# Kernel optimization log

Hardware: AMD Instinct MI355X
Metric: run time of the kernel (lower is better)

The kernel has to match this reference:

```python
import jax, jax.numpy as jnp
from jax import lax
import numpy as np

B, T, F, K = 64, 512, 1024, 64


def setup_inputs() -> dict:
    key = jax.random.key(0)
    ks = jax.random.split(key, 7)
    text_vec = jax.random.normal(ks[0], (B, T, F), dtype=jnp.float32)
    # variable-length mask; first timestep always on (torchcrf requirement)
    lengths = jax.random.randint(ks[1], (B,), T // 2, T + 1)
    mask = jnp.arange(T)[None, :] < lengths[:, None]  # [B,T] bool
    W = jax.random.normal(ks[2], (K, F), dtype=jnp.float32) * 0.02
    b = jnp.zeros((K,), dtype=jnp.float32)
    start_transitions = jax.random.uniform(ks[3], (K,), minval=-0.1, maxval=0.1)
    end_transitions = jax.random.uniform(ks[4], (K,), minval=-0.1, maxval=0.1)
    transitions = jax.random.uniform(ks[5], (K, K), minval=-0.1, maxval=0.1)
    return dict(text_vec=text_vec, mask=mask, W=W, b=b,
                start_transitions=start_transitions,
                end_transitions=end_transitions,
                transitions=transitions)


def _viterbi_decode(emission, mask, start, end, trans):
    """emission [N,T,K] float, mask [N,T] bool -> best tags [N,T] int32.
    Faithful masked Viterbi (torchcrf semantics); padded positions carry the
    last valid tag forward."""
    N, Tlen, Ktags = emission.shape
    score0 = start[None, :] + emission[:, 0]  # [N,K]
    idx_id = jnp.broadcast_to(jnp.arange(Ktags), (N, Ktags))

    def step(score, xs):
        e_t, m_t = xs  # [N,K], [N]
        cand = score[:, :, None] + trans[None, :, :] + e_t[:, None, :]  # [N,Kprev,Knext]
        new_score = jnp.max(cand, axis=1)
        best_prev = jnp.argmax(cand, axis=1)  # [N,K]
        new_score = jnp.where(m_t[:, None], new_score, score)
        best_prev = jnp.where(m_t[:, None], best_prev, idx_id)
        return new_score, best_prev

    xs = (jnp.swapaxes(emission[:, 1:], 0, 1), mask[:, 1:].T)  # time-major
    final_score, hist = lax.scan(step, score0, xs)  # hist [T-1,N,K]
    final_score = final_score + end[None, :]
    last_tag = jnp.argmax(final_score, axis=-1)  # [N]

    def back(tag, h_t):
        prev = jnp.take_along_axis(h_t, tag[:, None], axis=1)[:, 0]
        return prev, tag

    first_tag, tags_rest = lax.scan(back, last_tag, hist, reverse=True)
    tags = jnp.concatenate([first_tag[None, :], tags_rest], axis=0).T  # [N,T]
    return tags.astype(jnp.int32)


def reference(text_vec, mask, W, b, start_transitions, end_transitions, transitions):
    # cal_emission: Linear then reshape [B,T,K] -> [B,1,T,K]
    em = jnp.einsum('btf,kf->btk', text_vec, W) + b  # [B,T,K]
    emission = em[:, None, :, :]  # [B,1,T,K]
    # decode: flatten the singleton dim and run Viterbi
    em_flat = emission.reshape(-1, T, K)  # [B*1,T,K]
    mask_flat = jnp.broadcast_to(mask[:, None, :], (B, 1, T)).reshape(-1, T)
    pred = _viterbi_decode(em_flat, mask_flat, start_transitions,
                           end_transitions, transitions)
    pred = pred.reshape(B, 1, T)
    return emission, pred
```

## Files before the change

kernel.cpp:

```cpp
#include <hip/hip_runtime.h>
#include <hip/hip_bf16.h>

#define BB 64
#define TT 512
#define FF 1024
#define KK 64

typedef unsigned char uchar;
typedef float float2v __attribute__((ext_vector_type(2)));

#define BM 64
#define BF 64
#define LDA 68

__global__ __launch_bounds__(256)
void emission_kernel(const float* __restrict__ X, const float* __restrict__ W,
                     const float* __restrict__ bias, float* __restrict__ em)
{
    __shared__ float As[BF][LDA];
    __shared__ float Bs[BF][LDA];
    const int tid = threadIdx.x;
    const int row0 = blockIdx.x * BM;
    const int tm = tid & 15;
    const int tn = tid >> 4;
    const int lq = tid & 15;
    const int lr = tid >> 4;

    float acc[4][4];
#pragma unroll
    for (int i = 0; i < 4; ++i)
#pragma unroll
        for (int jj = 0; jj < 4; ++jj) acc[i][jj] = 0.f;

    for (int f0 = 0; f0 < FF; f0 += BF) {
#pragma unroll
        for (int p = 0; p < 4; ++p) {
            const int r = p * 16 + lr;
            float4 a = *(const float4*)(X + (size_t)(row0 + r) * FF + f0 + lq * 4);
            As[lq * 4 + 0][r] = a.x;
            As[lq * 4 + 1][r] = a.y;
            As[lq * 4 + 2][r] = a.z;
            As[lq * 4 + 3][r] = a.w;
            float4 w = *(const float4*)(W + (size_t)r * FF + f0 + lq * 4);
            Bs[lq * 4 + 0][r] = w.x;
            Bs[lq * 4 + 1][r] = w.y;
            Bs[lq * 4 + 2][r] = w.z;
            Bs[lq * 4 + 3][r] = w.w;
        }
        __syncthreads();
#pragma unroll
        for (int f = 0; f < BF; ++f) {
            float4 a = *(const float4*)&As[f][tm * 4];
            float4 b = *(const float4*)&Bs[f][tn * 4];
            acc[0][0] += a.x * b.x; acc[0][1] += a.x * b.y; acc[0][2] += a.x * b.z; acc[0][3] += a.x * b.w;
            acc[1][0] += a.y * b.x; acc[1][1] += a.y * b.y; acc[1][2] += a.y * b.z; acc[1][3] += a.y * b.w;
            acc[2][0] += a.z * b.x; acc[2][1] += a.z * b.y; acc[2][2] += a.z * b.z; acc[2][3] += a.z * b.w;
            acc[3][0] += a.w * b.x; acc[3][1] += a.w * b.y; acc[3][2] += a.w * b.z; acc[3][3] += a.w * b.w;
        }
        __syncthreads();
    }

    const float4 b4 = *(const float4*)(bias + tn * 4);
#pragma unroll
    for (int i = 0; i < 4; ++i) {
        float4 o;
        o.x = acc[i][0] + b4.x;
        o.y = acc[i][1] + b4.y;
        o.z = acc[i][2] + b4.z;
        o.w = acc[i][3] + b4.w;
        *(float4*)(em + (size_t)(row0 + tm * 4 + i) * KK + tn * 4) = o;
    }
}

#define VSTEP(EV, TIDX) do {                                                   \
    const float2v* sp2 = (const float2v*)&sbuf[(TIDX) & 1][0];                 \
    float m_;                                                                  \
    _Pragma("unroll")                                                          \
    for (int c = 0; c < 8; ++c) {                                              \
        const float2v p0 = sp2[c * 4 + 0] + tc2[c * 4 + 0];                    \
        const float2v p1 = sp2[c * 4 + 1] + tc2[c * 4 + 1];                    \
        const float2v p2 = sp2[c * 4 + 2] + tc2[c * 4 + 2];                    \
        const float2v p3 = sp2[c * 4 + 3] + tc2[c * 4 + 3];                    \
        const float ma = fmaxf(fmaxf(p0.x, p0.y), p1.x);           \
        const float mb = fmaxf(fmaxf(p1.y, p2.x), p2.y);                       \
        const float mc = fmaxf(fmaxf(p3.x, p3.y), ma);                         \
        const float w_ = fmaxf(mb, mc);                                        \
        m_ = (c == 0) ? w_ : fmaxf(m_, w_);                                    \
    }                                                                          \
    score = m_ + (EV);                                                         \
    sbuf[((TIDX) + 1) & 1][j] = score;       \
    sb[(size_t)(TIDX) * KK + j] = score;                                       \
} while (0)

#define RLANE(I) __uint_as_float((unsigned)__builtin_amdgcn_readlane((int)__float_as_uint(score), (I)))

__global__ __launch_bounds__(64)
__attribute__((amdgpu_waves_per_eu(1, 1)))
void viterbi_fwd(const float* __restrict__ em, const void* __restrict__ maskp,
                 const float* __restrict__ startT, const float* __restrict__ endT,
                 const float* __restrict__ trans, float* __restrict__ shist,
                 int* __restrict__ btarr)
{
    __shared__ float sbuf[2][KK];

    const int b = blockIdx.x;
    const int j = threadIdx.x;

    const uchar* m8 = (const uchar*)maskp;
    const int* m32 = (const int*)maskp;
    const bool u8m = (m8[1] != 0);

    int myc;
    if (u8m) {
        const uint2 mv = *(const uint2*)(m8 + (size_t)b * TT + j * 8);
        const unsigned s4 = (mv.x & 0x01010101u) + (mv.y & 0x01010101u);
        myc = (int)((s4 * 0x01010101u) >> 24);
    } else {
        const int* mp = m32 + (size_t)b * TT + j * 8;
        const int4 a = *(const int4*)mp;
        const int4 c = *(const int4*)(mp + 4);
        myc = (a.x != 0) + (a.y != 0) + (a.z != 0) + (a.w != 0)
            + (c.x != 0) + (c.y != 0) + (c.z != 0) + (c.w != 0);
    }
#pragma unroll
    for (int o = 1; o < 64; o <<= 1) myc += __shfl_xor(myc, o, 64);
    const int len = myc;

    float2v tc2[32];
#pragma unroll
    for (int i = 0; i < 32; ++i) {
        tc2[i].x = trans[(2 * i) * KK + j];
        tc2[i].y = trans[(2 * i + 1) * KK + j];
    }
#pragma unroll
    for (int i = 0; i < 32; ++i) asm volatile("" : "+v"(tc2[i]));

    const float* emb = em + (size_t)b * TT * KK;
    float* sb = shist + (size_t)b * TT * KK;

    float score = startT[j] + emb[j];
    sb[j] = score;
    sbuf[1][j] = score;

    float eA = emb[1 * KK + j];
    float eB = emb[2 * KK + j];
    float eC = emb[3 * KK + j];
    float eD = emb[4 * KK + j];

    int t = 1;
    for (; t + 3 < len; t += 4) {
        VSTEP(eA, t);     eA = emb[(size_t)((t + 4 < TT) ? t + 4 : TT - 1) * KK + j];
        VSTEP(eB, t + 1); eB = emb[(size_t)((t + 5 < TT) ? t + 5 : TT - 1) * KK + j];
        VSTEP(eC, t + 2); eC = emb[(size_t)((t + 6 < TT) ? t + 6 : TT - 1) * KK + j];
        VSTEP(eD, t + 3); eD = emb[(size_t)((t + 7 < TT) ? t + 7 : TT - 1) * KK + j];
    }
    for (; t < len; ++t) {
        VSTEP(eA, t);
        eA = eB; eB = eC; eC = eD;
    }

    score += endT[j];
    float bm = -__builtin_inff();
    int bt = 0;
#pragma unroll
    for (int i = 0; i < KK; ++i) {
        const float si = RLANE(i);
        if (si > bm) { bm = si; bt = i; }
    }
    if (j == 0) btarr[b] = bt;
}

__global__ __launch_bounds__(256)
void hist_kernel(const float* __restrict__ em, const void* __restrict__ maskp,
                 const float* __restrict__ trans, const float* __restrict__ shist,
                 uchar* __restrict__ histg)
{
    const int tid = threadIdx.x;
    const int bid = blockIdx.x;
    const int b = bid >> 6;
    const int t0 = (bid & 63) * 8;

    __shared__ float tl[64][65];
    __shared__ float srow[8][64];

    const uchar* m8 = (const uchar*)maskp;
    const int* m32 = (const int*)maskp;
    const bool u8m = (m8[1] != 0);

#pragma unroll
    for (int p = 0; p < 16; ++p) {
        const int idx = p * 256 + tid;
        tl[idx >> 6][idx & 63] = trans[idx];
    }
#pragma unroll
    for (int p = 0; p < 2; ++p) {
        const int idx = p * 256 + tid;
        const int r = idx >> 6, i2 = idx & 63;
        const int ts = t0 - 1 + r;
        srow[r][i2] = (ts >= 0) ? shist[((size_t)b * TT + ts) * KK + i2] : 0.f;
    }
    __syncthreads();

    const int j = tid & 63;
    const int tq = tid >> 6;

#pragma unroll
    for (int half = 0; half < 2; ++half) {
        const int toff = tq * 2 + half;
        const int t = t0 + toff;
        if (t == 0) continue;
        const int mt = u8m ? (int)m8[b * TT + t] : m32[b * TT + t];
        uchar hv;
        if (!mt) {
            hv = (uchar)j;
        } else {
            const float e = em[((size_t)b * TT + t) * KK + j];
            const float* sr = &srow[toff][0];
            float bm = -__builtin_inff();
            int bi = 0;
#pragma unroll 16
            for (int i = 0; i < KK; ++i) {
                const float cand = (sr[i] + tl[i][j]) + e;
                if (cand > bm) { bm = cand; bi = i; }
            }
            hv = (uchar)bi;
        }
        histg[((size_t)b * TT + t) * KK + j] = hv;
    }
}

__global__ __launch_bounds__(256)
void viterbi_bt(const uchar* __restrict__ histg, const int* __restrict__ btarr,
                float* __restrict__ pred)
{
    const int b = blockIdx.x;
    const int tid = threadIdx.x;
    const int w = tid >> 6;
    const int j = tid & 63;

    __shared__ uchar hist[TT][KK];
    __shared__ uchar hypo[8][64][64];

    const uint4* src = (const uint4*)(histg + (size_t)b * TT * KK);
    uint4* dst = (uint4*)&hist[0][0];
#pragma unroll
    for (int p = 0; p < 8; ++p) dst[p * 256 + tid] = src[p * 256 + tid];
    __syncthreads();

    const int bt = btarr[b];

#pragma unroll
    for (int ss = 0; ss < 2; ++ss) {
        const int s = w * 2 + ss;
        int tag = j;
        if (s == 7) {
            hypo[7][63][j] = (uchar)j;
            for (int t = TT - 1; t >= 7 * 64 + 1; --t) {
                tag = hist[t][tag];
                hypo[7][t - 1 - 7 * 64][j] = (uchar)tag;
            }
        } else {
            for (int t = (s + 1) * 64; t >= s * 64 + 1; --t) {
                tag = hist[t][tag];
                hypo[s][t - 1 - s * 64][j] = (uchar)tag;
            }
        }
    }
    __syncthreads();

    int rows_[8];
    rows_[7] = bt;
#pragma unroll
    for (int s = 6; s >= 0; --s) rows_[s] = hypo[s + 1][0][rows_[s + 1]];

    float* pb = pred + (size_t)b * TT;
#pragma unroll
    for (int ss = 0; ss < 2; ++ss) {
        const int s = w * 2 + ss;
        pb[s * 64 + j] = (float)hypo[s][j][rows_[s]];
    }
}

__global__ __launch_bounds__(256)
void viterbi_kernel(const float* __restrict__ em, const void* __restrict__ maskp,
                    const float* __restrict__ startT, const float* __restrict__ endT,
                    const float* __restrict__ trans, float* __restrict__ pred)
{
    const int b = blockIdx.x;
    const int tid = threadIdx.x;
    const int w = tid >> 6;
    const int j = tid & 63;

    __shared__ uchar hist[TT][KK];
    __shared__ uchar hypo[8][64][64];
    __shared__ int bt_sh;

    const uchar* m8 = (const uchar*)maskp;
    const int* m32 = (const int*)maskp;
    const bool u8m = (m8[1] != 0);

    if (w == 0) {
        float tc[KK];
#pragma unroll
        for (int i = 0; i < KK; ++i) tc[i] = trans[i * KK + j];

        const float* emb = em + (size_t)b * TT * KK;
        float score = startT[j] + emb[j];
        const float endv = endT[j];

        float e_cur = emb[KK + j];
        int   m_cur = u8m ? (int)m8[b * TT + 1] : m32[b * TT + 1];

        int t = 1;
        for (; t < TT; ++t) {
            const int tn2 = (t + 1 < TT) ? (t + 1) : (TT - 1);
            const float e_next = emb[(size_t)tn2 * KK + j];
            const int   m_next = u8m ? (int)m8[b * TT + tn2] : m32[b * TT + tn2];
            if (!m_cur) break;
            float m = -__builtin_inff();
            int idx = 0;
#pragma unroll
            for (int i = 0; i < KK; ++i) {
                const float si = __uint_as_float(__builtin_amdgcn_readlane(__float_as_uint(score), i));
                const float v = (si + tc[i]) + e_cur;
                if (v > m) { m = v; idx = i; }
            }
            score = m;
            hist[t][j] = (uchar)idx;
            e_cur = e_next; m_cur = m_next;
        }
        for (; t < TT; ++t) hist[t][j] = (uchar)j;

        score += endv;
        float bm = -__builtin_inff();
        int bt = 0;
#pragma unroll
        for (int i = 0; i < KK; ++i) {
            const float si = __uint_as_float(__builtin_amdgcn_readlane(__float_as_uint(score), i));
            if (si > bm) { bm = si; bt = i; }
        }
        if (j == 0) bt_sh = bt;
    }
    __syncthreads();

#pragma unroll
    for (int ss = 0; ss < 2; ++ss) {
        const int s = w * 2 + ss;
        int tag = j;
        if (s == 7) {
            hypo[7][63][j] = (uchar)j;
            for (int t = TT - 1; t >= 7 * 64 + 1; --t) {
                tag = hist[t][tag];
                hypo[7][t - 1 - 7 * 64][j] = (uchar)tag;
            }
        } else {
            for (int t = (s + 1) * 64; t >= s * 64 + 1; --t) {
                tag = hist[t][tag];
                hypo[s][t - 1 - s * 64][j] = (uchar)tag;
            }
        }
    }
    __syncthreads();

    const int bt = bt_sh;
    int rows_[8];
    rows_[7] = bt;
#pragma unroll
    for (int s = 6; s >= 0; --s) rows_[s] = hypo[s + 1][0][rows_[s + 1]];

    float* pb = pred + (size_t)b * TT;
#pragma unroll
    for (int ss = 0; ss < 2; ++ss) {
        const int s = w * 2 + ss;
        pb[s * 64 + j] = (float)hypo[s][j][rows_[s]];
    }
}

extern "C" void kernel_launch(void* const* d_in, const int* in_sizes, int n_in,
                              void* d_out, int out_size, void* d_ws, size_t ws_size,
                              hipStream_t stream) {
    const float* X      = (const float*)d_in[0];
    const void*  mask   = d_in[1];
    const float* W      = (const float*)d_in[2];
    const float* bias   = (const float*)d_in[3];
    const float* startT = (const float*)d_in[4];
    const float* endT   = (const float*)d_in[5];
    const float* trans  = (const float*)d_in[6];

    float* em   = (float*)d_out;
    float* pred = (float*)d_out + (size_t)BB * TT * KK;

    emission_kernel<<<(BB * TT) / BM, 256, 0, stream>>>(X, W, bias, em);

    const size_t SH_BYTES = (size_t)BB * TT * KK * sizeof(float);
    const size_t HI_BYTES = (size_t)BB * TT * KK;
    const size_t NEED = SH_BYTES + HI_BYTES + 256;

    if (ws_size >= NEED) {
        float* shist = (float*)d_ws;
        uchar* histg = (uchar*)d_ws + SH_BYTES;
        int*   btarr = (int*)((uchar*)d_ws + SH_BYTES + HI_BYTES);
        viterbi_fwd<<<BB, 64, 0, stream>>>(em, mask, startT, endT, trans, shist, btarr);
        hist_kernel<<<BB * 64, 256, 0, stream>>>(em, mask, trans, shist, histg);
        viterbi_bt<<<BB, 256, 0, stream>>>(histg, btarr, pred);
    } else {
        viterbi_kernel<<<BB, 256, 0, stream>>>(em, mask, startT, endT, trans, pred);
    }
}
```

Baseline: 218.9 us.

## Split-K emission GEMM with larger register tiles and separate reduction kernel

Result: faster. 200.1 us (-8.6%).

```diff
diff --git a/kernel.cpp b/kernel.cpp
--- a/kernel.cpp
+++ b/kernel.cpp
@@ -5,9 +5,109 @@
 #define TT 512
 #define FF 1024
 #define KK 64
+#define EMSZ ((size_t)BB * TT * KK)
 
 typedef unsigned char uchar;
 typedef float float2v __attribute__((ext_vector_type(2)));
+
+#define E3T 32
+#define E3PA 260
+#define E3PB 68
+
+__global__ __launch_bounds__(256)
+void emission3_kernel(const float* __restrict__ X, const float* __restrict__ W,
+                      float* __restrict__ part)
+{
+    __shared__ float As[E3T][E3PA];
+    __shared__ float Bs[E3T][E3PB];
+    const int tid = threadIdx.x;
+    const int bid = blockIdx.x;
+    const int fs = bid & 3;
+    const int rb = bid >> 2;
+    const int row0 = rb * 256;
+    const int fb = fs * 256;
+    const int rg = tid >> 3;
+    const int cg = tid & 7;
+    const int r_base = rg * 8;
+    const int c_base = cg * 8;
+
+    float acc[8][8];
+#pragma unroll
+    for (int i = 0; i < 8; ++i)
+#pragma unroll
+        for (int j = 0; j < 8; ++j) acc[i][j] = 0.f;
+
+    for (int ft = 0; ft < 256; ft += E3T) {
+#pragma unroll
+        for (int p = 0; p < 8; ++p) {
+            const int idx = p * 256 + tid;
+            const int row = idx >> 3;
+            const int fq = idx & 7;
+            const float4 a = *(const float4*)(X + (size_t)(row0 + row) * FF + fb + ft + fq * 4);
+            As[fq * 4 + 0][row] = a.x;
+            As[fq * 4 + 1][row] = a.y;
+            As[fq * 4 + 2][row] = a.z;
+            As[fq * 4 + 3][row] = a.w;
+        }
+#pragma unroll
+        for (int p = 0; p < 2; ++p) {
+            const int idx = p * 256 + tid;
+            const int c = idx >> 3;
+            const int fq = idx & 7;
+            const float4 w = *(const float4*)(W + (size_t)c * FF + fb + ft + fq * 4);
+            Bs[fq * 4 + 0][c] = w.x;
+            Bs[fq * 4 + 1][c] = w.y;
+            Bs[fq * 4 + 2][c] = w.z;
+            Bs[fq * 4 + 3][c] = w.w;
+        }
+        __syncthreads();
+#pragma unroll
+        for (int f = 0; f < E3T; ++f) {
+            const float4 a0 = *(const float4*)&As[f][r_base];
+            const float4 a1 = *(const float4*)&As[f][r_base + 4];
+            const float4 b0 = *(const float4*)&Bs[f][c_base];
+            const float4 b1 = *(const float4*)&Bs[f][c_base + 4];
+            const float av[8] = { a0.x, a0.y, a0.z, a0.w, a1.x, a1.y, a1.z, a1.w };
+            const float bv[8] = { b0.x, b0.y, b0.z, b0.w, b1.x, b1.y, b1.z, b1.w };
+#pragma unroll
+            for (int i = 0; i < 8; ++i)
+#pragma unroll
+                for (int j = 0; j < 8; ++j)
+                    acc[i][j] = fmaf(av[i], bv[j], acc[i][j]);
+        }
+        __syncthreads();
+    }
+
+    float* pp = part + (size_t)fs * EMSZ;
+#pragma unroll
+    for (int i = 0; i < 8; ++i) {
+        float4 o0, o1;
+        o0.x = acc[i][0]; o0.y = acc[i][1]; o0.z = acc[i][2]; o0.w = acc[i][3];
+        o1.x = acc[i][4]; o1.y = acc[i][5]; o1.z = acc[i][6]; o1.w = acc[i][7];
+        float* op = pp + (size_t)(row0 + r_base + i) * KK + c_base;
+        *(float4*)(op + 0) = o0;
+        *(float4*)(op + 4) = o1;
+    }
+}
+
+__global__ __launch_bounds__(256)
+void emadd_kernel(const float* __restrict__ part, const float* __restrict__ bias,
+                  float* __restrict__ em)
+{
+    const size_t i = (size_t)blockIdx.x * 256 + threadIdx.x;
+    const float4* p0 = (const float4*)part;
+    const float4* p1 = (const float4*)(part + EMSZ);
+    const float4* p2 = (const float4*)(part + 2 * EMSZ);
+    const float4* p3 = (const float4*)(part + 3 * EMSZ);
+    const float4 a = p0[i], b = p1[i], c = p2[i], d = p3[i];
+    const float4 bv = *(const float4*)(bias + ((int)(i & 15)) * 4);
+    float4 o;
+    o.x = (((a.x + b.x) + c.x) + d.x) + bv.x;
+    o.y = (((a.y + b.y) + c.y) + d.y) + bv.y;
+    o.z = (((a.z + b.z) + c.z) + d.z) + bv.z;
+    o.w = (((a.w + b.w) + c.w) + d.w) + bv.w;
+    ((float4*)em)[i] = o;
+}
 
 #define BM 64
 #define BF 64
@@ -88,7 +188,7 @@
         m_ = (c == 0) ? w_ : fmaxf(m_, w_);                                    \
     }                                                                          \
     score = m_ + (EV);                                                         \
-    sbuf[((TIDX) + 1) & 1][j] = score;       \
+    sbuf[((TIDX) + 1) & 1][j] = score;                                         \
     sb[(size_t)(TIDX) * KK + j] = score;                                       \
 } while (0)
 
@@ -388,22 +488,31 @@
     const float* trans  = (const float*)d_in[6];
 
     float* em   = (float*)d_out;
-    float* pred = (float*)d_out + (size_t)BB * TT * KK;
-
-    emission_kernel<<<(BB * TT) / BM, 256, 0, stream>>>(X, W, bias, em);
-
-    const size_t SH_BYTES = (size_t)BB * TT * KK * sizeof(float);
-    const size_t HI_BYTES = (size_t)BB * TT * KK;
-    const size_t NEED = SH_BYTES + HI_BYTES + 256;
+    float* pred = (float*)d_out + EMSZ;
+
+    const size_t SH_BYTES = EMSZ * sizeof(float);
+    const size_t HI_BYTES = EMSZ;
+    const size_t NEED  = SH_BYTES + HI_BYTES + 256;
+    const size_t P_OFF = NEED;
+    const size_t NEED3 = P_OFF + 4 * EMSZ * sizeof(float);
 
     if (ws_size >= NEED) {
         float* shist = (float*)d_ws;
         uchar* histg = (uchar*)d_ws + SH_BYTES;
         int*   btarr = (int*)((uchar*)d_ws + SH_BYTES + HI_BYTES);
+
+        if (ws_size >= NEED3) {
+            float* part = (float*)((uchar*)d_ws + P_OFF);
+            emission3_kernel<<<512, 256, 0, stream>>>(X, W, part);
+            emadd_kernel<<<(int)(EMSZ / 4 / 256), 256, 0, stream>>>(part, bias, em);
+        } else {
+            emission_kernel<<<(BB * TT) / BM, 256, 0, stream>>>(X, W, bias, em);
+        }
         viterbi_fwd<<<BB, 64, 0, stream>>>(em, mask, startT, endT, trans, shist, btarr);
         hist_kernel<<<BB * 64, 256, 0, stream>>>(em, mask, trans, shist, histg);
         viterbi_bt<<<BB, 256, 0, stream>>>(histg, btarr, pred);
     } else {
+        emission_kernel<<<(BB * TT) / BM, 256, 0, stream>>>(X, W, bias, em);
         viterbi_kernel<<<BB, 256, 0, stream>>>(em, mask, startT, endT, trans, pred);
     }
 }
```
